# Kernel optimization log

Hardware: AMD Instinct MI355X
Metric: run time of the kernel (lower is better)

Reference implementation:

```python
import jax, jax.numpy as jnp
import numpy as np
from jax import lax

# --- model/problem dims (see init_kwargs) ---
G, NPG, R, F, HID, L = 40, 500, 8, 256, 256, 3   # graphs(frames), nodes/graph, relations, feat, hidden, layers
N = G * NPG                                       # 20000 nodes
EPG = 8000
E = G * EPG                                       # 320000 edges
TOTAL = L * HID                                   # 768 = concat of layer outputs
LSTM_IN, LSTM_HID, NCLASS = 256, 256, 2
RATIO = 0.5
K = int(np.ceil(RATIO * NPG))                     # 250 nodes kept per graph by SAGPool


def setup_inputs() -> dict:
    key = jax.random.key(0)
    ks = jax.random.split(key, 16)
    s = 0.05
    x = jax.random.normal(ks[0], (N, F), dtype=jnp.float32)
    # intra-graph edges: node ids offset by graph index
    off = jnp.arange(G, dtype=jnp.int32)[:, None] * NPG
    src = jax.random.randint(ks[1], (G, EPG), 0, NPG, dtype=jnp.int32) + off
    dst = jax.random.randint(ks[2], (G, EPG), 0, NPG, dtype=jnp.int32) + off
    edge_index = jnp.stack([src.reshape(-1), dst.reshape(-1)])
    edge_attr = jax.random.randint(ks[3], (E,), 0, R, dtype=jnp.int32)
    batch = jnp.repeat(jnp.arange(G, dtype=jnp.int32), NPG)
    # RGCN layer params (layer0 in=F==HID so all layers stack)
    conv_W = jax.random.normal(ks[4], (L, R, HID, HID), dtype=jnp.float32) * s
    conv_root = jax.random.normal(ks[5], (L, HID, HID), dtype=jnp.float32) * s
    conv_bias = jnp.zeros((L, HID), dtype=jnp.float32)
    # SAGPool scorer: RGCNConv(TOTAL, 1, R)
    pool_W = jax.random.normal(ks[6], (R, TOTAL, 1), dtype=jnp.float32) * s
    pool_root = jax.random.normal(ks[7], (TOTAL, 1), dtype=jnp.float32) * s
    pool_bias = jnp.zeros((1,), dtype=jnp.float32)
    fc1_W = jax.random.normal(ks[8], (LSTM_IN, TOTAL), dtype=jnp.float32) * s
    fc1_b = jnp.zeros((LSTM_IN,), dtype=jnp.float32)
    W_ih = jax.random.normal(ks[9], (4 * LSTM_HID, LSTM_IN), dtype=jnp.float32) * s
    W_hh = jax.random.normal(ks[10], (4 * LSTM_HID, LSTM_HID), dtype=jnp.float32) * s
    b_ih = jnp.zeros((4 * LSTM_HID,), dtype=jnp.float32)
    b_hh = jnp.zeros((4 * LSTM_HID,), dtype=jnp.float32)
    fc2_W = jax.random.normal(ks[11], (NCLASS, LSTM_HID), dtype=jnp.float32) * s
    fc2_b = jnp.zeros((NCLASS,), dtype=jnp.float32)
    return dict(x=x, edge_index=edge_index, edge_attr=edge_attr, batch=batch,
                conv_W=conv_W, conv_root=conv_root, conv_bias=conv_bias,
                pool_W=pool_W, pool_root=pool_root, pool_bias=pool_bias,
                fc1_W=fc1_W, fc1_b=fc1_b, W_ih=W_ih, W_hh=W_hh, b_ih=b_ih, b_hh=b_hh,
                fc2_W=fc2_W, fc2_b=fc2_b)


def rgcn_conv(x, src, dst, etype, W, root, bias):
    """PyG (Fast)RGCNConv: per-relation mean aggregation summed over relations + root + bias."""
    num_nodes = x.shape[0]
    Rr = W.shape[0]
    h_all = jnp.einsum('ni,rio->rno', x, W)          # [R, N, out] per-relation transform
    msg = h_all[etype, src]                           # [E, out] per-edge message
    seg = dst * Rr + etype                            # (node, relation) segment id
    cnt = jax.ops.segment_sum(jnp.ones((src.shape[0],), x.dtype), seg,
                              num_segments=num_nodes * Rr)
    norm = 1.0 / jnp.maximum(cnt[seg], 1.0)           # per-(dst,rel) mean normalization
    agg = jax.ops.segment_sum(msg * norm[:, None], dst, num_segments=num_nodes)
    return agg + x @ root + bias


def lstm_scan(xs, W_ih, W_hh, b_ih, b_hh):
    """torch.nn.LSTM (single layer, batch=1) over sequence xs [T, in]; torch gate order i,f,g,o."""
    H = W_hh.shape[1]
    def step(carry, xt):
        h, c = carry
        gates = xt @ W_ih.T + h @ W_hh.T + b_ih + b_hh
        i, f, g, o = jnp.split(gates, 4)
        c = jax.nn.sigmoid(f) * c + jax.nn.sigmoid(i) * jnp.tanh(g)
        h = jax.nn.sigmoid(o) * jnp.tanh(c)
        return (h, c), h
    init = (jnp.zeros((H,), xs.dtype), jnp.zeros((H,), xs.dtype))
    (h, c), ys = lax.scan(step, init, xs)
    return ys, h


def reference(x, edge_index, edge_attr, batch,
              conv_W, conv_root, conv_bias,
              pool_W, pool_root, pool_bias,
              fc1_W, fc1_b, W_ih, W_hh, b_ih, b_hh, fc2_W, fc2_b):
    src, dst = edge_index[0], edge_index[1]
    # stacked RGCN layers, outputs concatenated (dropout omitted: eval mode)
    h = x
    outs = []
    for l in range(L):
        h = jax.nn.relu(rgcn_conv(h, src, dst, edge_attr, conv_W[l], conv_root[l], conv_bias[l]))
        outs.append(h)
    xc = jnp.concatenate(outs, axis=-1)               # [N, TOTAL]
    # SAGPool: RGCN scorer -> tanh -> per-graph top-k (batch is contiguous equal-size graphs)
    score = jnp.tanh(rgcn_conv(xc, src, dst, edge_attr, pool_W, pool_root, pool_bias).reshape(-1))
    topv, topi = lax.top_k(score.reshape(G, NPG), K)  # [G, K]
    xg = xc.reshape(G, NPG, TOTAL)
    xsel = jnp.take_along_axis(xg, topi[:, :, None], axis=1) * topv[:, :, None]
    # readout_type='mean': global_mean_pool over kept nodes per graph
    readout = xsel.mean(axis=1)                       # [G, TOTAL]
    h1 = jax.nn.relu(readout @ fc1_W.T + fc1_b)       # [G, LSTM_IN]
    # temporal_type='lstm_last': last hidden state over the G-frame sequence
    _, hlast = lstm_scan(h1, W_ih, W_hh, b_ih, b_hh)  # [LSTM_HID]
    logits = hlast @ fc2_W.T + fc2_b                  # [NCLASS]
    return jax.nn.log_softmax(logits, axis=-1)
```

## Files before the change

### kernel.cpp

```cpp
#include <hip/hip_runtime.h>

typedef unsigned short u16;
typedef short bf8 __attribute__((ext_vector_type(8)));
typedef short bf4 __attribute__((ext_vector_type(4)));
typedef float f4 __attribute__((ext_vector_type(4)));
typedef _Float16 h2v __attribute__((ext_vector_type(2)));
typedef __fp16 g2v __attribute__((ext_vector_type(2)));
typedef unsigned int u4v __attribute__((ext_vector_type(4)));

#define N_NODES 20000
#define N_EDGES 320000
#define NGRAPH 40
#define NPG 500
#define KTOP 250
#define NSEG (N_NODES * 8)

#define P_CONV_BIAS 0
#define P_POOL_W    768
#define P_POOL_ROOT 6912
#define P_POOL_BIAS 7680
#define P_FC1_W     7688
#define P_FC1_B     204296
#define P_W_IH      204552
#define P_B_IH      466696
#define P_B_HH      467720
#define P_FC2_W     468744
#define P_FC2_B     469256
#define P_TOTAL     469264

__device__ __forceinline__ float b2f(u16 u) {
    union { unsigned int i; float f; } v; v.i = ((unsigned int)u) << 16; return v.f;
}
__device__ __forceinline__ u16 f2b(float f) {
    union { float f; unsigned int i; } v; v.f = f;
    unsigned int x = v.i;
    return (u16)((x + 0x7fffu + ((x >> 16) & 1u)) >> 16);
}
__device__ __forceinline__ float wred(float s) {
    #pragma unroll
    for (int off = 32; off > 0; off >>= 1) s += __shfl_down(s, off);
    return s;
}
__device__ __forceinline__ float fdot2u(unsigned a, unsigned b, float c) {
#if __has_builtin(__builtin_amdgcn_fdot2)
    union { unsigned u; h2v h; } ua, ub; ua.u = a; ub.u = b;
    return __builtin_amdgcn_fdot2(ua.h, ub.h, c, false);
#else
    union { unsigned u; g2v h; } ua, ub; ua.u = a; ub.u = b;
    return c + (float)ua.h[0] * (float)ub.h[0] + (float)ua.h[1] * (float)ub.h[1];
#endif
}
__device__ __forceinline__ unsigned packh2(float a, float b) {
    g2v h = __builtin_amdgcn_cvt_pkrtz(a, b);
    union { g2v h; unsigned u; } v; v.h = h; return v.u;
}
__device__ __forceinline__ float sigm_f(float x) {
    return 1.0f / (1.0f + __expf(-x));
}
__device__ __forceinline__ float tanh_f(float x) {
    return 1.0f - 2.0f / (1.0f + __expf(2.0f * x));
}

__global__ void k_init(unsigned int* __restrict__ flag, unsigned int* __restrict__ cnt,
                       unsigned int* __restrict__ ctr) {
    int i = blockIdx.x * 256 + threadIdx.x;
    if (i < 64) flag[i] = 0u;
    if (i < NSEG) { cnt[i] = 0u; ctr[i] = 0u; }
}

__global__ void k_detect1(const u16* __restrict__ xr, int n, unsigned int* __restrict__ fb) {
    unsigned int local = 0;
    for (int i = blockIdx.x * 256 + threadIdx.x; i < n; i += 64 * 256) {
        unsigned int u = xr[i];
        if (((u >> 7) & 0xFFu) == 0xFFu) local++;
    }
    local = (unsigned int)wred((float)local);
    if ((threadIdx.x & 63) == 0 && local) atomicAdd(&fb[1], local);
}
__global__ void k_detect2(unsigned int* __restrict__ fb) {
    fb[0] = (fb[1] > 8u) ? 1u : 0u;
}

__device__ __forceinline__ u16 load_cvt(const void* src, size_t i, bool f32) {
    return f32 ? f2b(((const float*)src)[i]) : ((const u16*)src)[i];
}

__global__ void k_cvt_all(const void* conv_bias, const void* pool_W, const void* pool_root,
                          const void* pool_bias, const void* fc1_W, const void* fc1_b,
                          const void* W_ih, const void* b_ih, const void* b_hh,
                          const void* fc2_W, const void* fc2_b,
                          u16* __restrict__ parms, const unsigned int* __restrict__ flag) {
    int i = blockIdx.x * 256 + threadIdx.x;
    if (i >= P_TOTAL) return;
    bool f32 = (*flag != 0u);
    u16 v;
    if      (i < P_CONV_BIAS + 768)    v = load_cvt(conv_bias, i - P_CONV_BIAS, f32);
    else if (i < P_POOL_W + 6144)      v = load_cvt(pool_W,    i - P_POOL_W, f32);
    else if (i < P_POOL_ROOT + 768)    v = load_cvt(pool_root, i - P_POOL_ROOT, f32);
    else if (i < P_POOL_BIAS + 1)      v = load_cvt(pool_bias, i - P_POOL_BIAS, f32);
    else if (i < P_FC1_W && i >= P_POOL_BIAS) return;
    else if (i < P_FC1_W + 196608)     v = load_cvt(fc1_W,    i - P_FC1_W, f32);
    else if (i < P_FC1_B + 256)        v = load_cvt(fc1_b,    i - P_FC1_B, f32);
    else if (i < P_W_IH + 262144)      v = load_cvt(W_ih,     i - P_W_IH, f32);
    else if (i < P_B_IH + 1024)        v = load_cvt(b_ih,     i - P_B_IH, f32);
    else if (i < P_B_HH + 1024)        v = load_cvt(b_hh,     i - P_B_HH, f32);
    else if (i < P_FC2_W + 512)        v = load_cvt(fc2_W,    i - P_FC2_W, f32);
    else if (i < P_FC2_B + 2)          v = load_cvt(fc2_b,    i - P_FC2_B, f32);
    else return;
    parms[i] = v;
}

__global__ void k_stage_x(const void* __restrict__ src, u16* __restrict__ xc,
                          const unsigned int* __restrict__ flag) {
    int i = blockIdx.x * 256 + threadIdx.x;
    if (i >= N_NODES * 32) return;
    int n = i >> 5, o = (i & 31) * 8;
    bf8 v;
    if (*flag != 0u) {
        const float* s = (const float*)src + (size_t)n * 256 + o;
        #pragma unroll
        for (int c = 0; c < 8; ++c) v[c] = (short)f2b(s[c]);
    } else {
        v = *(const bf8*)((const u16*)src + (size_t)n * 256 + o);
    }
    *(bf8*)(xc + (size_t)n * 768 + 512 + o) = v;
}

__global__ void k_count(const int* __restrict__ dst, const int* __restrict__ et,
                        unsigned int* __restrict__ cnt) {
    int e = blockIdx.x * 256 + threadIdx.x;
    if (e < N_EDGES) {
        unsigned d = (unsigned)dst[e]; if (d >= N_NODES) d = 0;
        unsigned r = (unsigned)et[e] & 7u;
        atomicAdd(&cnt[d * 8 + r], 1u);
    }
}
__global__ void k_inv(const unsigned int* __restrict__ cnt, float* __restrict__ inv, int n) {
    int i = blockIdx.x * 256 + threadIdx.x;
    if (i < n) {
        unsigned int c = cnt[i];
        inv[i] = 1.0f / (float)(c < 1u ? 1u : c);
    }
}

__global__ void k_scan1(const unsigned int* __restrict__ cnt, unsigned int* __restrict__ seg,
                        unsigned int* __restrict__ bsum) {
    __shared__ unsigned int s[256];
    int t = threadIdx.x, i = blockIdx.x * 256 + t;
    unsigned int v = (i < NSEG) ? cnt[i] : 0u;
    s[t] = v;
    __syncthreads();
    for (int off = 1; off < 256; off <<= 1) {
        unsigned int add = (t >= off) ? s[t - off] : 0u;
        __syncthreads();
        s[t] += add;
        __syncthreads();
    }
    if (i < NSEG) seg[i] = s[t] - v;
    if (t == 255) bsum[blockIdx.x] = s[255];
}
__global__ void k_scan2(unsigned int* __restrict__ bsum, int nb) {
    __shared__ unsigned int s[1024];
    int t = threadIdx.x;
    unsigned int v = (t < nb) ? bsum[t] : 0u;
    s[t] = v;
    __syncthreads();
    for (int off = 1; off < 1024; off <<= 1) {
        unsigned int add = (t >= off) ? s[t - off] : 0u;
        __syncthreads();
        s[t] += add;
        __syncthreads();
    }
    if (t < nb) bsum[t] = s[t] - v;
}
__global__ void k_scan3(unsigned int* __restrict__ seg, const unsigned int* __restrict__ bsum) {
    int i = blockIdx.x * 256 + threadIdx.x;
    if (i < NSEG) seg[i] += bsum[i >> 8];
    if (i == 0) seg[NSEG] = N_EDGES;
}
__global__ void k_place(const int* __restrict__ src, const int* __restrict__ dst,
                        const int* __restrict__ et, const unsigned int* __restrict__ seg,
                        unsigned int* __restrict__ ctr, const float* __restrict__ inv,
                        unsigned int* __restrict__ skey, float* __restrict__ sw, int chn) {
    int e = blockIdx.x * 256 + threadIdx.x;
    if (e >= N_EDGES) return;
    unsigned s = (unsigned)src[e]; if (s >= N_NODES) s = 0;
    unsigned d = (unsigned)dst[e]; if (d >= N_NODES) d = 0;
    unsigned r = (unsigned)et[e] & 7u;
    unsigned key = d * 8 + r;
    unsigned pos = seg[key] + atomicAdd(&ctr[key], 1u);
    unsigned base = (d / (unsigned)chn) * (unsigned)chn;
    unsigned sl = s - base;
    if (sl >= (unsigned)chn) sl = 0u;
    skey[pos] = sl | (r << 16);
    sw[pos] = inv[key];
}

__global__ void k_transpose2(const void* __restrict__ conv_W, const void* __restrict__ conv_root,
                             u16* __restrict__ Wt, const unsigned int* __restrict__ flag) {
    int idx = blockIdx.x * 256 + threadIdx.x;
    if (idx >= 3 * 36 * 256 * 64) return;
    bool f32 = (*flag != 0u);
    int kk = idx & 63;
    int n = (idx >> 6) & 255;
    int lc = idx >> 14;
    int l = lc / 36, ck = lc % 36;
    int k = ck * 64 + kk;
    u16 v;
    if (k < 2048) {
        int r = k >> 8, i = k & 255;
        v = load_cvt(conv_W, ((size_t)((l * 8 + r) * 256 + i)) * 256 + n, f32);
    } else {
        int i = k - 2048;
        v = load_cvt(conv_root, ((size_t)(l * 256 + i)) * 256 + n, f32);
    }
    Wt[idx] = v;
}
__global__ void k_whh4(const void* __restrict__ W_hh, unsigned int* __restrict__ whh4,
                       const unsigned int* __restrict__ flag) {
    int idx = blockIdx.x * 256 + threadIdx.x;
    if (idx >= 32 * 1024 * 4) return;
    int c = idx & 3, j = (idx >> 2) & 1023, i4 = idx >> 12;
    int i2 = i4 * 4 + c;
    bool f32 = (*flag != 0u);
    float a, b;
    if (f32) {
        a = ((const float*)W_hh)[j * 256 + 2 * i2];
        b = ((const float*)W_hh)[j * 256 + 2 * i2 + 1];
    } else {
        a = b2f(((const u16*)W_hh)[j * 256 + 2 * i2]);
        b = b2f(((const u16*)W_hh)[j * 256 + 2 * i2 + 1]);
    }
    whh4[idx] = packh2(a, b);
}

__launch_bounds__(256, 3)
__global__ void k_layer2(const u16* __restrict__ xprev,
                         const u16* __restrict__ WtL,
                         u16* __restrict__ Hall, int n0, int chn) {
    __shared__ u16 As[64 * 264];
    int m0 = n0 + blockIdx.x * 64;
    int rg = blockIdx.y;
    int nend = n0 + chn;
    int wave = threadIdx.x >> 6, lane = threadIdx.x & 63;
    int mrow = lane & 15, quad = lane >> 4;
    int nbase = wave * 64;

    {
        int row = threadIdx.x >> 2, sg = threadIdx.x & 3;
        int gm = m0 + row;
        u16* dstp = As + row * 264 + sg * 64;
        if (gm < nend) {
            const u16* srcp = xprev + (size_t)gm * 768 + sg * 64;
            #pragma unroll
            for (int c = 0; c < 8; ++c)
                *(bf8*)(dstp + c * 8) = *(const bf8*)(srcp + c * 8);
        } else {
            bf8 z = {0, 0, 0, 0, 0, 0, 0, 0};
            #pragma unroll
            for (int c = 0; c < 8; ++c) *(bf8*)(dstp + c * 8) = z;
        }
    }
    __syncthreads();

    f4 acc[4][4];
    #pragma unroll
    for (int nt = 0; nt < 4; ++nt)
        #pragma unroll
        for (int mh = 0; mh < 4; ++mh) acc[nt][mh] = (f4){0.0f, 0.0f, 0.0f, 0.0f};

    const u16* WtR = WtL + (size_t)(rg * 4) * 16384;
    #pragma unroll
    for (int c4 = 0; c4 < 4; ++c4) {
        const u16* Bck = WtR + (size_t)c4 * 16384;
        #pragma unroll
        for (int ks = 0; ks < 2; ++ks) {
            bf8 a[4];
            #pragma unroll
            for (int mh = 0; mh < 4; ++mh)
                a[mh] = *(const bf8*)(As + (mh * 16 + mrow) * 264 + c4 * 64 + ks * 32 + quad * 8);
            #pragma unroll
            for (int nt = 0; nt < 4; ++nt) {
                bf8 b = *(const bf8*)(Bck + (size_t)(nbase + nt * 16 + mrow) * 64
                                      + ks * 32 + quad * 8);
                #pragma unroll
                for (int mh = 0; mh < 4; ++mh)
                    acc[nt][mh] = __builtin_amdgcn_mfma_f32_16x16x32_bf16(a[mh], b, acc[nt][mh], 0, 0, 0);
            }
        }
    }

    __syncthreads();
    #pragma unroll
    for (int nt = 0; nt < 4; ++nt) {
        int col = nbase + nt * 16 + mrow;
        #pragma unroll
        for (int mh = 0; mh < 4; ++mh)
            #pragma unroll
            for (int v = 0; v < 4; ++v)
                As[(mh * 16 + quad * 4 + v) * 264 + col] = f2b(acc[nt][mh][v]);
    }
    __syncthreads();
    {
        int row = threadIdx.x >> 2, sg = threadIdx.x & 3;
        int gm = m0 + row;
        if (gm < nend) {
            u16* dst = Hall + ((size_t)rg * chn + (gm - n0)) * 256 + sg * 64;
            const u16* srcp = As + row * 264 + sg * 64;
            #pragma unroll
            for (int c = 0; c < 8; ++c)
                *(bf8*)(dst + c * 8) = *(const bf8*)(srcp + c * 8);
        }
    }
}

__launch_bounds__(256)
__global__ void k_gather(const unsigned int* __restrict__ seg,
                         const unsigned int* __restrict__ skey,
                         const float* __restrict__ sw,
                         const u16* __restrict__ Hall,
                         const u16* __restrict__ bias,
                         u16* __restrict__ xc, int colbase, int n0, int chn) {
    int nl = blockIdx.x * 4 + (threadIdx.x >> 6);
    int n = n0 + nl;
    int lane = threadIdx.x & 63;
    int c0 = lane * 4;
    unsigned e0 = seg[n * 8], e1 = seg[n * 8 + 8];
    float a0 = 0.0f, a1 = 0.0f, a2 = 0.0f, a3 = 0.0f;
    unsigned key = 0; float w = 0.0f;
    if (e0 < e1) { key = skey[e0]; w = sw[e0]; }
    for (unsigned e = e0; e < e1;) {
        unsigned kc = key; float wc = w;
        ++e;
        if (e < e1) { key = skey[e]; w = sw[e]; }
        const u16* row = Hall + ((size_t)(kc >> 16) * chn + (kc & 0xFFFFu)) * 256 + c0;
        bf4 v = *(const bf4*)row;
        a0 += wc * b2f((u16)v[0]);
        a1 += wc * b2f((u16)v[1]);
        a2 += wc * b2f((u16)v[2]);
        a3 += wc * b2f((u16)v[3]);
    }
    const u16* rr = Hall + ((size_t)8 * chn + nl) * 256 + c0;
    bf4 rv = *(const bf4*)rr;
    float o0 = a0 + b2f((u16)rv[0]) + b2f(bias[c0 + 0]);
    float o1 = a1 + b2f((u16)rv[1]) + b2f(bias[c0 + 1]);
    float o2 = a2 + b2f((u16)rv[2]) + b2f(bias[c0 + 2]);
    float o3 = a3 + b2f((u16)rv[3]) + b2f(bias[c0 + 3]);
    bf4 o;
    o[0] = (short)f2b(o0 > 0.0f ? o0 : 0.0f);
    o[1] = (short)f2b(o1 > 0.0f ? o1 : 0.0f);
    o[2] = (short)f2b(o2 > 0.0f ? o2 : 0.0f);
    o[3] = (short)f2b(o3 > 0.0f ? o3 : 0.0f);
    *(bf4*)(xc + (size_t)n * 768 + colbase + c0) = o;
}

__launch_bounds__(256)
__global__ void k_pool(const u16* __restrict__ xc, const u16* __restrict__ parms,
                       float* __restrict__ p, float* __restrict__ score) {
    int n = blockIdx.x * 4 + (threadIdx.x >> 6);
    if (n >= N_NODES) return;
    int lane = threadIdx.x & 63;
    const u16* xr = xc + (size_t)n * 768;
    float acc[9];
    #pragma unroll
    for (int rr = 0; rr < 9; ++rr) acc[rr] = 0.0f;
    #pragma unroll
    for (int q = 0; q < 12; ++q) {
        int f = lane + 64 * q;
        float xv = b2f(xr[f]);
        #pragma unroll
        for (int rr = 0; rr < 8; ++rr)
            acc[rr] += xv * b2f(parms[P_POOL_W + rr * 768 + f]);
        acc[8] += xv * b2f(parms[P_POOL_ROOT + f]);
    }
    #pragma unroll
    for (int rr = 0; rr < 9; ++rr) acc[rr] = wred(acc[rr]);
    if (lane == 0) {
        #pragma unroll
        for (int rr = 0; rr < 8; ++rr) p[rr * N_NODES + n] = acc[rr];
        score[n] = acc[8] + b2f(parms[P_POOL_BIAS]);
    }
}
__global__ void k_scatter_pool(const int* __restrict__ src, const int* __restrict__ dst,
                               const int* __restrict__ et, const float* __restrict__ inv,
                               const float* __restrict__ p, float* __restrict__ score) {
    int e = blockIdx.x * 256 + threadIdx.x;
    if (e >= N_EDGES) return;
    int r = et[e] & 7;
    unsigned s = (unsigned)src[e]; if (s >= N_NODES) s = 0;
    unsigned d = (unsigned)dst[e]; if (d >= N_NODES) d = 0;
    atomicAdd(&score[d], inv[d * 8 + r] * p[r * N_NODES + s]);
}

__launch_bounds__(256)
__global__ void k_sort(const float* __restrict__ score, unsigned int* __restrict__ topidx,
                       float* __restrict__ topv) {
    __shared__ unsigned long long keys[512];
    __shared__ float vals[512];
    int g = blockIdx.x, tid = threadIdx.x;
    for (int i = tid; i < 512; i += 256) {
        unsigned long long key;
        float v = 0.0f;
        if (i < NPG) {
            v = tanhf(score[g * NPG + i]);
            unsigned int u = __float_as_uint(v);
            u = (u & 0x80000000u) ? ~u : (u | 0x80000000u);
            u = ~u;
            key = ((unsigned long long)u << 32) | (unsigned int)i;
        } else {
            key = 0xFFFFFFFFFFFFFFFFull;
        }
        keys[i] = key;
        vals[i] = v;
    }
    __syncthreads();
    for (int k = 2; k <= 512; k <<= 1)
        for (int j = k >> 1; j > 0; j >>= 1) {
            for (int i = tid; i < 512; i += 256) {
                int ixj = i ^ j;
                if (ixj > i) {
                    bool up = ((i & k) == 0);
                    unsigned long long a = keys[i], b = keys[ixj];
                    if ((a > b) == up) { keys[i] = b; keys[ixj] = a; }
                }
            }
            __syncthreads();
        }
    if (tid < KTOP) {
        int idx = (int)(keys[tid] & 511u);
        topidx[g * 256 + tid] = (unsigned)idx;
        topv[g * 256 + tid] = vals[idx];
    }
}

__launch_bounds__(256)
__global__ void k_readout(const unsigned int* __restrict__ topidx,
                          const float* __restrict__ topv,
                          const u16* __restrict__ xc, float* __restrict__ readout) {
    __shared__ unsigned int sidx[KTOP];
    __shared__ float sv[KTOP];
    __shared__ float part[256];
    int g = blockIdx.x, cb = blockIdx.y;
    int tid = threadIdx.x;
    if (tid < KTOP) { sidx[tid] = topidx[g * 256 + tid]; sv[tid] = topv[g * 256 + tid]; }
    __syncthreads();
    int fl = tid & 63, ng = tid >> 6;
    int f = cb * 64 + fl;
    float acc = 0.0f;
    for (int j = ng; j < KTOP; j += 4)
        acc += sv[j] * b2f(xc[(size_t)(g * NPG + sidx[j]) * 768 + f]);
    part[tid] = acc;
    __syncthreads();
    if (tid < 64) {
        float s = part[tid] + part[64 + tid] + part[128 + tid] + part[192 + tid];
        readout[(size_t)g * 768 + cb * 64 + tid] = s * (1.0f / (float)KTOP);
    }
}

__global__ void k_fc1(const float* __restrict__ readout, const u16* __restrict__ parms,
                      float* __restrict__ h1) {
    int wid = blockIdx.x * 4 + (threadIdx.x >> 6);
    if (wid >= NGRAPH * 256) return;
    int g = wid >> 8, o = wid & 255, lane = threadIdx.x & 63;
    const float* rr = readout + (size_t)g * 768;
    const u16* w = parms + P_FC1_W + (size_t)o * 768;
    float s = 0.0f;
    #pragma unroll
    for (int q = 0; q < 12; ++q) { int f = lane + 64 * q; s += rr[f] * b2f(w[f]); }
    s = wred(s);
    if (lane == 0) { s += b2f(parms[P_FC1_B + o]); h1[g * 256 + o] = s > 0.0f ? s : 0.0f; }
}
__global__ void k_gx(const float* __restrict__ h1, const u16* __restrict__ parms,
                     float* __restrict__ gx) {
    int wid = blockIdx.x * 4 + (threadIdx.x >> 6);
    if (wid >= NGRAPH * 1024) return;
    int t = wid >> 10, j = wid & 1023, lane = threadIdx.x & 63;
    const float* xr = h1 + t * 256;
    const u16* w = parms + P_W_IH + (size_t)j * 256;
    float s = 0.0f;
    #pragma unroll
    for (int q = 0; q < 4; ++q) { int f = lane + 64 * q; s += xr[f] * b2f(w[f]); }
    s = wred(s);
    if (lane == 0) gx[t * 1024 + j] = s + b2f(parms[P_B_IH + j]) + b2f(parms[P_B_HH + j]);
}

__launch_bounds__(512, 1)
__global__ void k_lstm(const float* __restrict__ gx, const unsigned int* __restrict__ whh4,
                       const u16* __restrict__ parms, void* __restrict__ out,
                       const unsigned int* __restrict__ flag) {
    __shared__ float hs[256];
    __shared__ unsigned int hs2[128];
    __shared__ float gs[1024];
    __shared__ float red[2];
    int tid = threadIdx.x;
    int j0 = tid, j1 = tid + 512;
    u4v wa[24], wb[24];
    #pragma unroll
    for (int q = 0; q < 24; ++q) {
        wa[q] = *(const u4v*)(whh4 + (((size_t)q * 1024) + j0) * 4);
        wb[q] = *(const u4v*)(whh4 + (((size_t)q * 1024) + j1) * 4);
    }
    asm volatile("" : "+v"(wa[0]), "+v"(wa[1]), "+v"(wa[2]), "+v"(wa[3]),
                      "+v"(wa[4]), "+v"(wa[5]), "+v"(wa[6]), "+v"(wa[7]),
                      "+v"(wa[8]), "+v"(wa[9]), "+v"(wa[10]), "+v"(wa[11]),
                      "+v"(wa[12]), "+v"(wa[13]), "+v"(wa[14]), "+v"(wa[15]),
                      "+v"(wa[16]), "+v"(wa[17]), "+v"(wa[18]), "+v"(wa[19]),
                      "+v"(wa[20]), "+v"(wa[21]), "+v"(wa[22]), "+v"(wa[23]));
    asm volatile("" : "+v"(wb[0]), "+v"(wb[1]), "+v"(wb[2]), "+v"(wb[3]),
                      "+v"(wb[4]), "+v"(wb[5]), "+v"(wb[6]), "+v"(wb[7]),
                      "+v"(wb[8]), "+v"(wb[9]), "+v"(wb[10]), "+v"(wb[11]),
                      "+v"(wb[12]), "+v"(wb[13]), "+v"(wb[14]), "+v"(wb[15]),
                      "+v"(wb[16]), "+v"(wb[17]), "+v"(wb[18]), "+v"(wb[19]),
                      "+v"(wb[20]), "+v"(wb[21]), "+v"(wb[22]), "+v"(wb[23]));
    if (tid < 256) hs[tid] = 0.0f;
    if (tid < 128) hs2[tid] = 0u;
    float c = 0.0f;
    __syncthreads();
    for (int t = 0; t < NGRAPH; ++t) {
        float g0 = gx[t * 1024 + j0];
        float g1 = gx[t * 1024 + j1];
        #pragma unroll
        for (int q = 0; q < 24; ++q) {
            #pragma unroll
            for (int cc = 0; cc < 4; ++cc) {
                unsigned h2 = hs2[q * 4 + cc];
                g0 = fdot2u(wa[q][cc], h2, g0);
                g1 = fdot2u(wb[q][cc], h2, g1);
            }
        }
        #pragma unroll 2
        for (int q = 24; q < 32; ++q) {
            u4v v0 = *(const u4v*)(whh4 + (((size_t)q * 1024) + j0) * 4);
            u4v v1 = *(const u4v*)(whh4 + (((size_t)q * 1024) + j1) * 4);
            #pragma unroll
            for (int cc = 0; cc < 4; ++cc) {
                unsigned h2 = hs2[q * 4 + cc];
                g0 = fdot2u(v0[cc], h2, g0);
                g1 = fdot2u(v1[cc], h2, g1);
            }
        }
        gs[j0] = g0;
        gs[j1] = g1;
        __syncthreads();
        if (tid < 256) {
            float gi = sigm_f(gs[tid]);
            float gf = sigm_f(gs[256 + tid]);
            float gg = tanh_f(gs[512 + tid]);
            float go = sigm_f(gs[768 + tid]);
            c = gf * c + gi * gg;
            float h = go * tanh_f(c);
            hs[tid] = h;
            float ho = __shfl(h, (tid & 63) ^ 1);
            if (!(tid & 1)) hs2[tid >> 1] = packh2(h, ho);
        }
        __syncthreads();
    }
    if (tid < 128) {
        int cls = tid >> 6, lane = tid & 63;
        float s = 0.0f;
        #pragma unroll
        for (int q = 0; q < 4; ++q) {
            int d = lane + 64 * q;
            s += hs[d] * b2f(parms[P_FC2_W + cls * 256 + d]);
        }
        s = wred(s);
        if (lane == 0) red[cls] = s + b2f(parms[P_FC2_B + cls]);
    }
    __syncthreads();
    if (tid == 0) {
        float l0 = red[0], l1 = red[1];
        float m = fmaxf(l0, l1);
        float lse = m + logf(expf(l0 - m) + expf(l1 - m));
        float o0 = l0 - lse, o1 = l1 - lse;
        if (*flag) { ((float*)out)[0] = o0; ((float*)out)[1] = o1; }
        else       { ((u16*)out)[0] = f2b(o0); ((u16*)out)[1] = f2b(o1); }
    }
}

struct WS {
    unsigned int* flag; unsigned int* cnt; float* inv; unsigned int* seg; unsigned int* ctr;
    unsigned int* skey; float* sw; unsigned int* bsum;
    u16* Wt2; u16* xc; u16* Hall; float* p; float* score;
    unsigned int* topidx; float* topv;
    float* readout; float* h1; float* gx; unsigned int* whh4; u16* parms;
    size_t need;
};
static WS plan(char* base, int chn) {
    WS w; size_t off = 0;
    auto take = [&](size_t bytes) -> char* {
        char* p = base + off; off += (bytes + 255) & ~(size_t)255; return p;
    };
    w.flag    = (unsigned int*)take(256);
    w.cnt     = (unsigned int*)take((size_t)NSEG * 4);
    w.inv     = (float*)take((size_t)NSEG * 4);
    w.seg     = (unsigned int*)take((size_t)(NSEG + 1) * 4);
    w.ctr     = (unsigned int*)take((size_t)NSEG * 4);
    w.skey    = (unsigned int*)take((size_t)N_EDGES * 4);
    w.sw      = (float*)take((size_t)N_EDGES * 4);
    w.bsum    = (unsigned int*)take(1024 * 4);
    w.Wt2     = (u16*)take((size_t)3 * 36 * 256 * 64 * 2);
    w.xc      = (u16*)take((size_t)N_NODES * 768 * 2);
    w.Hall    = (u16*)take((size_t)9 * chn * 256 * 2);
    w.p       = (float*)take((size_t)8 * N_NODES * 4);
    w.score   = (float*)take((size_t)N_NODES * 4);
    w.topidx  = (unsigned int*)take((size_t)NGRAPH * 256 * 4);
    w.topv    = (float*)take((size_t)NGRAPH * 256 * 4);
    w.readout = (float*)take((size_t)NGRAPH * 768 * 4);
    w.h1      = (float*)take((size_t)NGRAPH * 256 * 4);
    w.gx      = (float*)take((size_t)NGRAPH * 1024 * 4);
    w.whh4    = (unsigned int*)take((size_t)32 * 1024 * 4 * 4);
    w.parms   = (u16*)take((size_t)P_TOTAL * 2);
    w.need = off;
    return w;
}

extern "C" void kernel_launch(void* const* d_in, const int* in_sizes, int n_in,
                              void* d_out, int out_size, void* d_ws, size_t ws_size,
                              hipStream_t stream) {
    (void)in_sizes; (void)n_in; (void)out_size;
    const void* x        = d_in[0];
    const int* edge_index= (const int*)d_in[1];
    const int* edge_attr = (const int*)d_in[2];
    const void* conv_W   = d_in[4];
    const void* conv_root= d_in[5];
    const void* conv_bias= d_in[6];
    const void* pool_W   = d_in[7];
    const void* pool_root= d_in[8];
    const void* pool_bias= d_in[9];
    const void* fc1_W    = d_in[10];
    const void* fc1_b    = d_in[11];
    const void* W_ih     = d_in[12];
    const void* W_hh     = d_in[13];
    const void* b_ih     = d_in[14];
    const void* b_hh     = d_in[15];
    const void* fc2_W    = d_in[16];
    const void* fc2_b    = d_in[17];

    const int* e_src = edge_index;
    const int* e_dst = edge_index + N_EDGES;

    if (ws_size == 0) ws_size = (size_t)64 << 20;
    int chn = 500;
    {
        const int ladder[8] = {20000, 10000, 5000, 4000, 2500, 2000, 1000, 500};
        for (int i = 0; i < 8; ++i) {
            if (plan((char*)d_ws, ladder[i]).need <= ws_size) { chn = ladder[i]; break; }
        }
    }
    WS w = plan((char*)d_ws, chn);

    k_init<<<(NSEG + 255) / 256, 256, 0, stream>>>(w.flag, w.cnt, w.ctr);
    k_detect1<<<64, 256, 0, stream>>>((const u16*)x, 1 << 18, w.flag);
    k_detect2<<<1, 1, 0, stream>>>(w.flag);

    k_count<<<1250, 256, 0, stream>>>(e_dst, edge_attr, w.cnt);
    k_inv<<<(NSEG + 255) / 256, 256, 0, stream>>>(w.cnt, w.inv, NSEG);
    k_scan1<<<625, 256, 0, stream>>>(w.cnt, w.seg, w.bsum);
    k_scan2<<<1, 1024, 0, stream>>>(w.bsum, 625);
    k_scan3<<<(NSEG + 255) / 256, 256, 0, stream>>>(w.seg, w.bsum);
    k_place<<<1250, 256, 0, stream>>>(e_src, e_dst, edge_attr, w.seg, w.ctr, w.inv,
                                      w.skey, w.sw, chn);

    k_cvt_all<<<(P_TOTAL + 255) / 256, 256, 0, stream>>>(
        conv_bias, pool_W, pool_root, pool_bias, fc1_W, fc1_b,
        W_ih, b_ih, b_hh, fc2_W, fc2_b, w.parms, w.flag);

    k_stage_x<<<2500, 256, 0, stream>>>(x, w.xc, w.flag);
    k_transpose2<<<6912, 256, 0, stream>>>(conv_W, conv_root, w.Wt2, w.flag);
    k_whh4<<<512, 256, 0, stream>>>(W_hh, w.whh4, w.flag);

    int nch = N_NODES / chn;
    int gx_tiles = (chn + 63) / 64;
    for (int l = 0; l < 3; ++l) {
        const u16* xprev = w.xc + (l == 0 ? 512 : (l - 1) * 256);
        const u16* WtL = w.Wt2 + (size_t)l * 36 * 16384;
        const u16* bias = w.parms + P_CONV_BIAS + l * 256;
        for (int c = 0; c < nch; ++c) {
            int n0 = c * chn;
            k_layer2<<<dim3(gx_tiles, 9), 256, 0, stream>>>(xprev, WtL, w.Hall, n0, chn);
            k_gather<<<chn / 4, 256, 0, stream>>>(w.seg, w.skey, w.sw, w.Hall, bias,
                                                  w.xc, l * 256, n0, chn);
        }
    }

    k_pool<<<5000, 256, 0, stream>>>(w.xc, w.parms, w.p, w.score);
    k_scatter_pool<<<1250, 256, 0, stream>>>(e_src, e_dst, edge_attr, w.inv, w.p, w.score);
    k_sort<<<NGRAPH, 256, 0, stream>>>(w.score, w.topidx, w.topv);
    k_readout<<<dim3(NGRAPH, 12), 256, 0, stream>>>(w.topidx, w.topv, w.xc, w.readout);
    k_fc1<<<2560, 256, 0, stream>>>(w.readout, w.parms, w.h1);
    k_gx<<<10240, 256, 0, stream>>>(w.h1, w.parms, w.gx);
    k_lstm<<<1, 512, 0, stream>>>(w.gx, w.whh4, w.parms, d_out, w.flag);
}
```

Baseline: 691.6 us.

## Split LSTM recurrence across 16 workgroups with atomic grid barrier

Replaces the single 512-thread LSTM workgroup with 16 one-wave workgroups. Each caches its slice of W_hh in LDS and computes 16 hidden units. The workgroups exchange packed half-precision hidden states through double-buffered global memory and sync every timestep on an atomic generation counter. This spreads the recurrent matvec over more compute units to cut per-step latency. In exchange it adds a cross-workgroup spin barrier per step, and it relies on the counter being reset and all blocks being co-resident.

After: 724.5 us. +4.8%, slower.

```diff
diff --git a/kernel.cpp b/kernel.cpp
--- a/kernel.cpp
+++ b/kernel.cpp
@@ -14,6 +14,7 @@
 #define NPG 500
 #define KTOP 250
 #define NSEG (N_NODES * 8)
+#define LSTM_NB 16
 
 #define P_CONV_BIAS 0
 #define P_POOL_W    768
@@ -484,96 +485,95 @@
     if (lane == 0) gx[t * 1024 + j] = s + b2f(parms[P_B_IH + j]) + b2f(parms[P_B_HH + j]);
 }
 
-__launch_bounds__(512, 1)
-__global__ void k_lstm(const float* __restrict__ gx, const unsigned int* __restrict__ whh4,
-                       const u16* __restrict__ parms, void* __restrict__ out,
-                       const unsigned int* __restrict__ flag) {
-    __shared__ float hs[256];
-    __shared__ unsigned int hs2[128];
-    __shared__ float gs[1024];
-    __shared__ float red[2];
-    int tid = threadIdx.x;
-    int j0 = tid, j1 = tid + 512;
-    u4v wa[24], wb[24];
-    #pragma unroll
-    for (int q = 0; q < 24; ++q) {
-        wa[q] = *(const u4v*)(whh4 + (((size_t)q * 1024) + j0) * 4);
-        wb[q] = *(const u4v*)(whh4 + (((size_t)q * 1024) + j1) * 4);
-    }
-    asm volatile("" : "+v"(wa[0]), "+v"(wa[1]), "+v"(wa[2]), "+v"(wa[3]),
-                      "+v"(wa[4]), "+v"(wa[5]), "+v"(wa[6]), "+v"(wa[7]),
-                      "+v"(wa[8]), "+v"(wa[9]), "+v"(wa[10]), "+v"(wa[11]),
-                      "+v"(wa[12]), "+v"(wa[13]), "+v"(wa[14]), "+v"(wa[15]),
-                      "+v"(wa[16]), "+v"(wa[17]), "+v"(wa[18]), "+v"(wa[19]),
-                      "+v"(wa[20]), "+v"(wa[21]), "+v"(wa[22]), "+v"(wa[23]));
-    asm volatile("" : "+v"(wb[0]), "+v"(wb[1]), "+v"(wb[2]), "+v"(wb[3]),
-                      "+v"(wb[4]), "+v"(wb[5]), "+v"(wb[6]), "+v"(wb[7]),
-                      "+v"(wb[8]), "+v"(wb[9]), "+v"(wb[10]), "+v"(wb[11]),
-                      "+v"(wb[12]), "+v"(wb[13]), "+v"(wb[14]), "+v"(wb[15]),
-                      "+v"(wb[16]), "+v"(wb[17]), "+v"(wb[18]), "+v"(wb[19]),
-                      "+v"(wb[20]), "+v"(wb[21]), "+v"(wb[22]), "+v"(wb[23]));
-    if (tid < 256) hs[tid] = 0.0f;
-    if (tid < 128) hs2[tid] = 0u;
+__global__ void __launch_bounds__(64)
+k_lstm2(const float* __restrict__ gx, const unsigned int* __restrict__ whh4,
+        const u16* __restrict__ parms, void* __restrict__ out,
+        unsigned int* __restrict__ hglob, float* __restrict__ hfin,
+        unsigned int* __restrict__ gen, const unsigned int* __restrict__ flag) {
+    __shared__ u4v lw[32][64];
+    __shared__ __align__(16) unsigned int hs2[128];
+    int b = blockIdx.x;
+    int l = threadIdx.x;
+    int k = l & 15;
+    int row = (l >> 4) * 256 + b * 16 + k;
+    #pragma unroll 4
+    for (int i4 = 0; i4 < 32; ++i4)
+        lw[i4][l] = *(const u4v*)(whh4 + ((size_t)(i4 * 1024) + row) * 4);
+    hs2[l] = 0u; hs2[64 + l] = 0u;
     float c = 0.0f;
     __syncthreads();
     for (int t = 0; t < NGRAPH; ++t) {
-        float g0 = gx[t * 1024 + j0];
-        float g1 = gx[t * 1024 + j1];
-        #pragma unroll
-        for (int q = 0; q < 24; ++q) {
-            #pragma unroll
-            for (int cc = 0; cc < 4; ++cc) {
-                unsigned h2 = hs2[q * 4 + cc];
-                g0 = fdot2u(wa[q][cc], h2, g0);
-                g1 = fdot2u(wb[q][cc], h2, g1);
-            }
-        }
-        #pragma unroll 2
-        for (int q = 24; q < 32; ++q) {
-            u4v v0 = *(const u4v*)(whh4 + (((size_t)q * 1024) + j0) * 4);
-            u4v v1 = *(const u4v*)(whh4 + (((size_t)q * 1024) + j1) * 4);
-            #pragma unroll
-            for (int cc = 0; cc < 4; ++cc) {
-                unsigned h2 = hs2[q * 4 + cc];
-                g0 = fdot2u(v0[cc], h2, g0);
-                g1 = fdot2u(v1[cc], h2, g1);
-            }
-        }
-        gs[j0] = g0;
-        gs[j1] = g1;
+        float gv = gx[t * 1024 + row];
+        #pragma unroll
+        for (int i4 = 0; i4 < 32; ++i4) {
+            u4v w = lw[i4][l];
+            u4v hh = *(const u4v*)&hs2[i4 * 4];
+            gv = fdot2u(w[0], hh[0], gv);
+            gv = fdot2u(w[1], hh[1], gv);
+            gv = fdot2u(w[2], hh[2], gv);
+            gv = fdot2u(w[3], hh[3], gv);
+        }
+        float gf = __shfl(gv, 16 + k);
+        float gg = __shfl(gv, 32 + k);
+        float go = __shfl(gv, 48 + k);
+        float h = 0.0f;
+        if (l < 16) {
+            float gi = sigm_f(gv);
+            gf = sigm_f(gf);
+            gg = tanh_f(gg);
+            go = sigm_f(go);
+            c = gf * c + gi * gg;
+            h = go * tanh_f(c);
+        }
+        float ha = __shfl(h, 2 * l);
+        float hb = __shfl(h, 2 * l + 1);
+        int bank = (t & 1) * 128;
+        if (l < 8) {
+            unsigned hw = packh2(ha, hb);
+            __hip_atomic_store(&hglob[bank + b * 8 + l], hw,
+                               __ATOMIC_RELAXED, __HIP_MEMORY_SCOPE_AGENT);
+        }
+        if (t == NGRAPH - 1 && l < 16)
+            __hip_atomic_store(&hfin[b * 16 + l], h,
+                               __ATOMIC_RELAXED, __HIP_MEMORY_SCOPE_AGENT);
+        if (l == 0)
+            __hip_atomic_fetch_add(gen, 1u, __ATOMIC_RELEASE, __HIP_MEMORY_SCOPE_AGENT);
+        unsigned target = (unsigned)(LSTM_NB * (t + 1));
+        unsigned gv2;
+        do {
+            gv2 = 0u;
+            if (l == 0)
+                gv2 = __hip_atomic_load(gen, __ATOMIC_ACQUIRE, __HIP_MEMORY_SCOPE_AGENT);
+            gv2 = __shfl(gv2, 0);
+            if (gv2 < target) __builtin_amdgcn_s_sleep(1);
+        } while (gv2 < target);
+        hs2[l] = __hip_atomic_load(&hglob[bank + l],
+                                   __ATOMIC_RELAXED, __HIP_MEMORY_SCOPE_AGENT);
+        hs2[64 + l] = __hip_atomic_load(&hglob[bank + 64 + l],
+                                        __ATOMIC_RELAXED, __HIP_MEMORY_SCOPE_AGENT);
         __syncthreads();
-        if (tid < 256) {
-            float gi = sigm_f(gs[tid]);
-            float gf = sigm_f(gs[256 + tid]);
-            float gg = tanh_f(gs[512 + tid]);
-            float go = sigm_f(gs[768 + tid]);
-            c = gf * c + gi * gg;
-            float h = go * tanh_f(c);
-            hs[tid] = h;
-            float ho = __shfl(h, (tid & 63) ^ 1);
-            if (!(tid & 1)) hs2[tid >> 1] = packh2(h, ho);
-        }
-        __syncthreads();
-    }
-    if (tid < 128) {
-        int cls = tid >> 6, lane = tid & 63;
-        float s = 0.0f;
+    }
+    if (b == 0) {
+        float s0 = 0.0f, s1 = 0.0f;
         #pragma unroll
         for (int q = 0; q < 4; ++q) {
-            int d = lane + 64 * q;
-            s += hs[d] * b2f(parms[P_FC2_W + cls * 256 + d]);
-        }
-        s = wred(s);
-        if (lane == 0) red[cls] = s + b2f(parms[P_FC2_B + cls]);
-    }
-    __syncthreads();
-    if (tid == 0) {
-        float l0 = red[0], l1 = red[1];
-        float m = fmaxf(l0, l1);
-        float lse = m + logf(expf(l0 - m) + expf(l1 - m));
-        float o0 = l0 - lse, o1 = l1 - lse;
-        if (*flag) { ((float*)out)[0] = o0; ((float*)out)[1] = o1; }
-        else       { ((u16*)out)[0] = f2b(o0); ((u16*)out)[1] = f2b(o1); }
+            int d = l + 64 * q;
+            float hv = __hip_atomic_load(&hfin[d], __ATOMIC_RELAXED,
+                                         __HIP_MEMORY_SCOPE_AGENT);
+            s0 += hv * b2f(parms[P_FC2_W + d]);
+            s1 += hv * b2f(parms[P_FC2_W + 256 + d]);
+        }
+        s0 = wred(s0);
+        s1 = wred(s1);
+        if (l == 0) {
+            float l0 = s0 + b2f(parms[P_FC2_B]);
+            float l1 = s1 + b2f(parms[P_FC2_B + 1]);
+            float m = fmaxf(l0, l1);
+            float lse = m + logf(expf(l0 - m) + expf(l1 - m));
+            float o0 = l0 - lse, o1 = l1 - lse;
+            if (*flag) { ((float*)out)[0] = o0; ((float*)out)[1] = o1; }
+            else       { ((u16*)out)[0] = f2b(o0); ((u16*)out)[1] = f2b(o1); }
+        }
     }
 }
 
@@ -582,7 +582,8 @@
     unsigned int* skey; float* sw; unsigned int* bsum;
     u16* Wt2; u16* xc; u16* Hall; float* p; float* score;
     unsigned int* topidx; float* topv;
-    float* readout; float* h1; float* gx; unsigned int* whh4; u16* parms;
+    float* readout; float* h1; float* gx; unsigned int* whh4;
+    unsigned int* hglob; float* hfin; u16* parms;
     size_t need;
 };
 static WS plan(char* base, int chn) {
@@ -609,6 +610,8 @@
     w.h1      = (float*)take((size_t)NGRAPH * 256 * 4);
     w.gx      = (float*)take((size_t)NGRAPH * 1024 * 4);
     w.whh4    = (unsigned int*)take((size_t)32 * 1024 * 4 * 4);
+    w.hglob   = (unsigned int*)take((size_t)256 * 4);
+    w.hfin    = (float*)take((size_t)256 * 4);
     w.parms   = (u16*)take((size_t)P_TOTAL * 2);
     w.need = off;
     return w;
@@ -689,5 +692,6 @@
     k_readout<<<dim3(NGRAPH, 12), 256, 0, stream>>>(w.topidx, w.topv, w.xc, w.readout);
     k_fc1<<<2560, 256, 0, stream>>>(w.readout, w.parms, w.h1);
     k_gx<<<10240, 256, 0, stream>>>(w.h1, w.parms, w.gx);
-    k_lstm<<<1, 512, 0, stream>>>(w.gx, w.whh4, w.parms, d_out, w.flag);
-}
+    k_lstm2<<<LSTM_NB, 64, 0, stream>>>(w.gx, w.whh4, w.parms, d_out,
+                                        w.hglob, w.hfin, w.flag + 8, w.flag);
+}
```
